# Optimization experiments

Measured on AMD Instinct MI355X. Metric: run time of the kernel, lower is better.

## Reference

```python
import jax, jax.numpy as jnp
import numpy as np


def setup_inputs() -> dict:
    key = jax.random.key(0)
    k1, k2, k3, k4, k5 = jax.random.split(key, 5)
    b, c, l, h, w = 16, 64, 8, 56, 56
    cl = c * l
    return {
        "inpt": jax.random.normal(k1, (b, c, l, h, w), dtype=jnp.float32),
        "theta_w": jax.random.normal(k2, (cl,), dtype=jnp.float32) * (1.0 / np.sqrt(cl)),
        "g_w": jax.random.normal(k3, (cl,), dtype=jnp.float32) * (1.0 / np.sqrt(cl)),
        "h_w": jax.random.normal(k4, (cl,), dtype=jnp.float32),
        "h_b": jax.random.normal(k5, (cl,), dtype=jnp.float32) * 0.1,
    }


def reference(inpt, theta_w, g_w, h_w, h_b):
    # inpt: [b, c, l, h, w] -> flatten channel/time to cl and space to n = h*w
    b, c, l, h, w = inpt.shape
    cl, n = c * l, h * w
    x = inpt.reshape(b, cl, n)  # [b, cl, n]

    # 1x1 convs (bias=False) projecting cl -> 1 channel
    t = jnp.einsum("bcn,c->bn", x, theta_w)  # theta(inpt): [b, n]
    g = jnp.einsum("bcn,c->bn", x, g_w)      # g(inpt):     [b, n]

    # torch: outer product t (b,1,n) * g^T (b,n,1) -> [b,n,n], AvgPool1d(n) over last dim
    # mathematically: att[b,i] = g[b,i] * mean_j t[b,j]
    att = g * jnp.mean(t, axis=1, keepdims=True)  # [b, n]

    # h: 1x1 conv 1 -> cl channels with bias, then residual add
    out = x + att[:, None, :] * h_w[None, :, None] + h_b[None, :, None]  # [b, cl, n]
    return out.reshape(b, cl, h, w)
```

## Files before the change

### kernel.cpp

```cpp
#include <hip/hip_runtime.h>

#define BATCH 16
#define CL    512
#define NSP   3136
#define N4    (NSP / 4)
#define CHUNK 32
#define NCHUNK ((N4 + CHUNK - 1) / CHUNK)
#define GROUPS 8
#define CPG   (CL / GROUPS)

typedef float nfloat4 __attribute__((ext_vector_type(4)));

__global__ __launch_bounds__(256) void sa_pass1(
    const float* __restrict__ x,
    const float* __restrict__ theta_w,
    const float* __restrict__ g_w,
    float* __restrict__ g_out,
    float* __restrict__ t_part)
{
    const int b     = blockIdx.x;
    const int chunk = blockIdx.y;
    const int tid   = threadIdx.x;
    const int tx    = tid & 31;
    const int gq    = tid >> 5;
    const int i4    = chunk * CHUNK + tx;
    const bool valid = (i4 < N4);

    const float4* xb = (const float4*)x + (size_t)b * CL * N4;

    float4 gv = make_float4(0.f, 0.f, 0.f, 0.f);
    float4 tv = make_float4(0.f, 0.f, 0.f, 0.f);
    if (valid) {
        const int c0 = gq * CPG;
        #pragma unroll 4
        for (int c = c0; c < c0 + CPG; ++c) {
            float4 xv = xb[(size_t)c * N4 + i4];
            float gw = g_w[c];
            float tw = theta_w[c];
            gv.x += xv.x * gw; gv.y += xv.y * gw;
            gv.z += xv.z * gw; gv.w += xv.w * gw;
            tv.x += xv.x * tw; tv.y += xv.y * tw;
            tv.z += xv.z * tw; tv.w += xv.w * tw;
        }
    }

    __shared__ float4 sg[GROUPS][CHUNK];
    __shared__ float4 st[GROUPS][CHUNK];
    sg[gq][tx] = gv;
    st[gq][tx] = tv;
    __syncthreads();

    if (tid < 32) {
        float4 G = sg[0][tx];
        float4 T = st[0][tx];
        #pragma unroll
        for (int k = 1; k < GROUPS; ++k) {
            float4 a  = sg[k][tx];
            float4 t2 = st[k][tx];
            G.x += a.x;  G.y += a.y;  G.z += a.z;  G.w += a.w;
            T.x += t2.x; T.y += t2.y; T.z += t2.z; T.w += t2.w;
        }
        if (valid)
            ((float4*)g_out)[(size_t)b * N4 + i4] = G;

        float s = T.x + T.y + T.z + T.w;
        #pragma unroll
        for (int off = 16; off > 0; off >>= 1)
            s += __shfl_down(s, off, 32);
        if (tx == 0)
            t_part[b * NCHUNK + chunk] = s;
    }
}

#define P2_F4_PER_BLOCK 512
__global__ __launch_bounds__(256) void sa_pass2(
    const float* __restrict__ x,
    const float* __restrict__ g_arr,
    const float* __restrict__ t_part,
    const float* __restrict__ h_w,
    const float* __restrict__ h_b,
    float* __restrict__ out)
{
    const int blk = blockIdx.x;
    const int b   = blk / ((CL * N4) / P2_F4_PER_BLOCK);

    __shared__ float sm;
    if (threadIdx.x < 32) {
        float v = (threadIdx.x < NCHUNK) ? t_part[b * NCHUNK + threadIdx.x] : 0.f;
        #pragma unroll
        for (int off = 16; off > 0; off >>= 1)
            v += __shfl_down(v, off, 32);
        if (threadIdx.x == 0)
            sm = v * (1.0f / (float)NSP);
    }
    __syncthreads();
    const float m = sm;

    const size_t base = (size_t)blk * P2_F4_PER_BLOCK + threadIdx.x;
    #pragma unroll
    for (int r = 0; r < P2_F4_PER_BLOCK / 256; ++r) {
        const size_t f = base + (size_t)r * 256;
        const int i4 = (int)(f % N4);
        const int bc = (int)(f / N4);
        const int c  = bc & (CL - 1);

        float4 xv = ((const float4*)x)[f];
        float4 gv = ((const float4*)g_arr)[(size_t)b * N4 + i4];
        const float hw = h_w[c];
        const float hb = h_b[c];
        const float mh = m * hw;

        nfloat4 o;
        o.x = xv.x + mh * gv.x + hb;
        o.y = xv.y + mh * gv.y + hb;
        o.z = xv.z + mh * gv.z + hb;
        o.w = xv.w + mh * gv.w + hb;
        __builtin_nontemporal_store(o, (nfloat4*)out + f);
    }
}

extern "C" void kernel_launch(void* const* d_in, const int* in_sizes, int n_in,
                              void* d_out, int out_size, void* d_ws, size_t ws_size,
                              hipStream_t stream)
{
    const float* x       = (const float*)d_in[0];
    const float* theta_w = (const float*)d_in[1];
    const float* g_w     = (const float*)d_in[2];
    const float* h_w     = (const float*)d_in[3];
    const float* h_b     = (const float*)d_in[4];
    float* out = (float*)d_out;

    float* t_ws = (float*)d_ws;
    float* g_ws = (float*)((char*)d_ws + 2048);

    dim3 grid1(BATCH, NCHUNK);
    sa_pass1<<<grid1, 256, 0, stream>>>(x, theta_w, g_w, g_ws, t_ws);

    const int total4 = BATCH * CL * N4;
    sa_pass2<<<total4 / P2_F4_PER_BLOCK, 256, 0, stream>>>(x, g_ws, t_ws, h_w, h_b, out);
}
```

Before: 200.4 us.

## Split pass1 into narrower spatial chunks with more channel groups, enlarge pass2 blocks

Pass1 now handles 8 float4 columns per block and splits the channels into 32 groups instead of 8, which launches about 4x more blocks to fill the GPU. The partial sums are combined with a two-stage shared-memory reduction. The channel loop is fully unrolled so more loads are in flight per thread. Pass2 processes 1024 float4 per block and reduces the now 98 partial t-sums with two wavefronts; the workspace offset for g grows to fit the extra partials. The cost is shorter contiguous runs per row in pass1 (128-byte segments), which may hurt coalescing.

Result: no change. 203.7 us (+1.7%).

```diff
diff --git a/kernel.cpp b/kernel.cpp
--- a/kernel.cpp
+++ b/kernel.cpp
@@ -4,9 +4,9 @@
 #define CL    512
 #define NSP   3136
 #define N4    (NSP / 4)
-#define CHUNK 32
-#define NCHUNK ((N4 + CHUNK - 1) / CHUNK)
-#define GROUPS 8
+#define CHUNK 8
+#define NCHUNK (N4 / CHUNK)
+#define GROUPS 32
 #define CPG   (CL / GROUPS)
 
 typedef float nfloat4 __attribute__((ext_vector_type(4)));
@@ -21,18 +21,17 @@
     const int b     = blockIdx.x;
     const int chunk = blockIdx.y;
     const int tid   = threadIdx.x;
-    const int tx    = tid & 31;
-    const int gq    = tid >> 5;
+    const int tx    = tid & (CHUNK - 1);
+    const int gq    = tid >> 3;
     const int i4    = chunk * CHUNK + tx;
-    const bool valid = (i4 < N4);
 
     const float4* xb = (const float4*)x + (size_t)b * CL * N4;
 
     float4 gv = make_float4(0.f, 0.f, 0.f, 0.f);
     float4 tv = make_float4(0.f, 0.f, 0.f, 0.f);
-    if (valid) {
+    {
         const int c0 = gq * CPG;
-        #pragma unroll 4
+        #pragma unroll
         for (int c = c0; c < c0 + CPG; ++c) {
             float4 xv = xb[(size_t)c * N4 + i4];
             float gw = g_w[c];
@@ -50,29 +49,45 @@
     st[gq][tx] = tv;
     __syncthreads();
 
-    if (tid < 32) {
-        float4 G = sg[0][tx];
-        float4 T = st[0][tx];
+    if (tid < 64) {
+        const int lx = tid & (CHUNK - 1);
+        const int k  = tid >> 3;
+        float4 G = sg[k][lx];
+        float4 T = st[k][lx];
         #pragma unroll
-        for (int k = 1; k < GROUPS; ++k) {
-            float4 a  = sg[k][tx];
-            float4 t2 = st[k][tx];
+        for (int s = 8; s < GROUPS; s += 8) {
+            float4 a  = sg[k + s][lx];
+            float4 t2 = st[k + s][lx];
             G.x += a.x;  G.y += a.y;  G.z += a.z;  G.w += a.w;
             T.x += t2.x; T.y += t2.y; T.z += t2.z; T.w += t2.w;
         }
-        if (valid)
-            ((float4*)g_out)[(size_t)b * N4 + i4] = G;
+        sg[k][lx] = G;
+        st[k][lx] = T;
+    }
+    __syncthreads();
+
+    if (tid < CHUNK) {
+        float4 G = sg[0][tid];
+        float4 T = st[0][tid];
+        #pragma unroll
+        for (int k = 1; k < 8; ++k) {
+            float4 a  = sg[k][tid];
+            float4 t2 = st[k][tid];
+            G.x += a.x;  G.y += a.y;  G.z += a.z;  G.w += a.w;
+            T.x += t2.x; T.y += t2.y; T.z += t2.z; T.w += t2.w;
+        }
+        ((float4*)g_out)[(size_t)b * N4 + chunk * CHUNK + tid] = G;
 
         float s = T.x + T.y + T.z + T.w;
         #pragma unroll
-        for (int off = 16; off > 0; off >>= 1)
-            s += __shfl_down(s, off, 32);
-        if (tx == 0)
+        for (int off = 4; off > 0; off >>= 1)
+            s += __shfl_down(s, off, 8);
+        if (tid == 0)
             t_part[b * NCHUNK + chunk] = s;
     }
 }
 
-#define P2_F4_PER_BLOCK 512
+#define P2_F4_PER_BLOCK 1024
 __global__ __launch_bounds__(256) void sa_pass2(
     const float* __restrict__ x,
     const float* __restrict__ g_arr,
@@ -84,19 +99,24 @@
     const int blk = blockIdx.x;
     const int b   = blk / ((CL * N4) / P2_F4_PER_BLOCK);
 
+    __shared__ float red[2];
     __shared__ float sm;
-    if (threadIdx.x < 32) {
-        float v = (threadIdx.x < NCHUNK) ? t_part[b * NCHUNK + threadIdx.x] : 0.f;
+    const int tid = threadIdx.x;
+    if (tid < 128) {
+        float v = (tid < NCHUNK) ? t_part[b * NCHUNK + tid] : 0.f;
         #pragma unroll
-        for (int off = 16; off > 0; off >>= 1)
-            v += __shfl_down(v, off, 32);
-        if (threadIdx.x == 0)
-            sm = v * (1.0f / (float)NSP);
+        for (int off = 32; off > 0; off >>= 1)
+            v += __shfl_down(v, off, 64);
+        if ((tid & 63) == 0)
+            red[tid >> 6] = v;
     }
+    __syncthreads();
+    if (tid == 0)
+        sm = (red[0] + red[1]) * (1.0f / (float)NSP);
     __syncthreads();
     const float m = sm;
 
-    const size_t base = (size_t)blk * P2_F4_PER_BLOCK + threadIdx.x;
+    const size_t base = (size_t)blk * P2_F4_PER_BLOCK + tid;
     #pragma unroll
     for (int r = 0; r < P2_F4_PER_BLOCK / 256; ++r) {
         const size_t f = base + (size_t)r * 256;
@@ -131,7 +151,7 @@
     float* out = (float*)d_out;
 
     float* t_ws = (float*)d_ws;
-    float* g_ws = (float*)((char*)d_ws + 2048);
+    float* g_ws = (float*)((char*)d_ws + 8192);
 
     dim3 grid1(BATCH, NCHUNK);
     sa_pass1<<<grid1, 256, 0, stream>>>(x, theta_w, g_w, g_ws, t_ws);
```
